# Kernel optimization log

Hardware: AMD Instinct MI355X
Metric: run time of the kernel (lower is better)

The kernel has to match this reference:

```python
import jax, jax.numpy as jnp
import numpy as np
import math

B, N, K, M = 8, 512, 128, 100

def _lin(k, fi, fo):
    kw, kb = jax.random.split(k)
    return (jax.random.normal(kw, (fi, fo), jnp.float32) / np.sqrt(fi).astype(np.float32),
            jax.random.normal(kb, (fo,), jnp.float32) * 0.01)

def setup_inputs() -> dict:
    key = jax.random.key(0)
    ks = jax.random.split(key, 10)
    xyz = jax.random.uniform(ks[0], (B, N, K, 3), jnp.float32, minval=0.5, maxval=2.8)
    counts = jax.random.randint(ks[1], (B, N), 32, K + 1)
    # padded neighbor list: valid neighbors first (flag=1), padding zeros after -> break == mask
    flags = (jnp.arange(K)[None, None, :] < counts[:, :, None]).astype(jnp.float32)
    image_dR = jnp.concatenate([xyz, flags[..., None]], axis=-1)  # [B,N,K,4]
    ew0, eb0 = _lin(ks[2], 1, 25)
    ew1, eb1 = _lin(ks[3], 25, 50)
    ew2, eb2 = _lin(ks[4], 50, M)
    fw0, fb0 = _lin(ks[5], 16 * M, 240)
    fw1, fb1 = _lin(ks[6], 240, 240)
    fw2, fb2 = _lin(ks[7], 240, 240)
    fw3, fb3 = _lin(ks[8], 240, 1)
    return dict(image_dR=image_dR, ew0=ew0, eb0=eb0, ew1=ew1, eb1=eb1, ew2=ew2, eb2=eb2,
                fw0=fw0, fb0=fb0, fw1=fw1, fb1=fb1, fw2=fw2, fb2=fb2, fw3=fw3, fb3=fb3)

def reference(image_dR, ew0, eb0, ew1, eb1, ew2, eb2, fw0, fb0, fw1, fb1, fw2, fb2, fw3, fb3):
    list_neigh = image_dR[..., 3]            # [B,N,K] neighbor flag
    xyz = image_dR[..., :3]                  # [B,N,K,3]
    Rij = jnp.sum(xyz * xyz, axis=-1)        # NOTE: original overwrites sqrt -> squared distance
    mask = list_neigh > 0
    lt10 = Rij < 10.0
    b1 = mask & lt10
    b2 = (~lt10) & (Rij < 25.0)              # cosine branch ignores mask (faithful)
    safe = jnp.where(Rij == 0.0, 1.0, Rij)
    S = jnp.where(b1, 1.0 / safe,
                  jnp.where(b2, 0.5 * jnp.cos(math.pi * (Rij - 10.0) / 15.0) + 0.5, 0.0))
    coef = jnp.where(mask, S / safe, 0.0)    # per-neighbor scaling for xyz channels
    Ri = jnp.concatenate([S[..., None], coef[..., None] * xyz], axis=-1)  # [B,N,K,4]
    # embedding net on scalar S_Rij
    h = jnp.tanh(S[..., None] @ ew0 + eb0)
    h = jnp.tanh(h @ ew1 + eb1)
    G = jnp.tanh(h @ ew2 + eb2)              # [B,N,K,M]
    G16 = G[..., :16]
    tmpA = jnp.einsum('bnjm,bnjf->bnmf', G16, Ri)   # [B,N,16,4]
    tmpB = jnp.einsum('bnjf,bnjm->bnfm', Ri, G)     # [B,N,4,M]
    DR = jnp.einsum('bnmf,bnfh->bnmh', tmpA, tmpB).reshape(image_dR.shape[0], image_dR.shape[1], -1)
    h = jnp.tanh(DR @ fw0 + fb0)
    h = jnp.tanh(h @ fw1 + fb1)
    h = jnp.tanh(h @ fw2 + fb2)
    Ei = h @ fw3 + fb3                       # [B,N,1]
    Etot = jnp.sum(Ei, axis=1)               # [B,1]
    return Etot, Ei
```

## Files before the change

kernel.cpp:

```cpp
#include <hip/hip_runtime.h>
#include <hip/hip_bf16.h>
#include <math.h>

#define B_ 8
#define N_ 512
#define K_ 128
#define M_ 100
#define NPAIR (B_*N_)
#define DRLEN 1600
#define F0 240
#define NPAD 256

#define NLUT 2048
#define LUT_STRIDE 128
#define SMAX 1.5f
#define EPB 8

using bf16x8 = __attribute__((ext_vector_type(8))) __bf16;
using f32x4  = __attribute__((ext_vector_type(4))) float;

static __device__ __forceinline__ float tanh_f(float x){
  float xc = fminf(fmaxf(x, -15.f), 15.f);
  float e = __expf(2.f*xc);
  return __fdividef(e - 1.f, e + 1.f);
}

__global__ __launch_bounds__(256) void lut_build_par(
    const float* __restrict__ ew0, const float* __restrict__ eb0,
    const float* __restrict__ ew1, const float* __restrict__ eb1,
    const float* __restrict__ ew2, const float* __restrict__ eb2,
    float* __restrict__ T)
{
  __shared__ float sh0[EPB][26];
  __shared__ float sh1[EPB][52];
  const int e0 = blockIdx.x * EPB;
  const int t = threadIdx.x;

  if (t < EPB*25){
    int e = t / 25, c = t % 25;
    float S = (float)(e0 + e) * (SMAX / (float)(NLUT - 1));
    sh0[e][c] = tanh_f(fmaf(S, ew0[c], eb0[c]));
  }
  __syncthreads();

  for (int o = t; o < EPB*50; o += 256){
    int e = o / 50, c = o % 50;
    float a = eb1[c], b = 0.f;
    #pragma unroll
    for (int k = 0; k < 24; k += 2){
      a = fmaf(sh0[e][k],   ew1[k*50 + c],     a);
      b = fmaf(sh0[e][k+1], ew1[(k+1)*50 + c], b);
    }
    a = fmaf(sh0[e][24], ew1[24*50 + c], a);
    sh1[e][c] = tanh_f(a + b);
  }
  __syncthreads();

  for (int o = t; o < EPB*M_; o += 256){
    int e = o / M_, c = o % M_;
    float a = eb2[c], b = 0.f;
    #pragma unroll
    for (int k = 0; k < 50; k += 2){
      a = fmaf(sh1[e][k],   ew2[k*M_ + c],     a);
      b = fmaf(sh1[e][k+1], ew2[(k+1)*M_ + c], b);
    }
    T[(size_t)(e0 + e)*LUT_STRIDE + c] = tanh_f(a + b);
  }
}

__global__ __launch_bounds__(256) void prep_w0t(
    const float* __restrict__ src, __hip_bfloat16* __restrict__ dst)
{
  __shared__ float tile[64][65];
  const int k0 = blockIdx.x * 64;
  const int n0 = blockIdx.y * 64;
  const int tc = threadIdx.x & 63, tr = threadIdx.x >> 6;

  #pragma unroll
  for (int i = 0; i < 16; i += 1){
    int r = i*4 + tr;
    int n = n0 + tc;
    tile[r][tc] = (n < F0) ? src[(size_t)(k0 + r)*F0 + n] : 0.f;
  }
  __syncthreads();
  #pragma unroll
  for (int i = 0; i < 16; i += 1){
    int r = i*4 + tr;
    dst[(size_t)(n0 + r)*DRLEN + k0 + tc] = __float2bfloat16(tile[tc][r]);
  }
}

__global__ __launch_bounds__(256) void prep_small(
    const float* __restrict__ fw1, const float* __restrict__ fw2,
    const float* __restrict__ fb0, const float* __restrict__ fb1,
    const float* __restrict__ fb2,
    __hip_bfloat16* __restrict__ W1T, __hip_bfloat16* __restrict__ W2T,
    float* __restrict__ b0p, float* __restrict__ b1p, float* __restrict__ b2p)
{
  int idx = blockIdx.x*256 + threadIdx.x;
  if (idx < NPAD*NPAD){
    int n = idx / NPAD, k = idx % NPAD;
    W1T[idx] = __float2bfloat16((n < F0 && k < F0) ? fw1[(size_t)k*F0 + n] : 0.f);
  } else if (idx < 2*NPAD*NPAD){
    int j = idx - NPAD*NPAD;
    int n = j / NPAD, k = j % NPAD;
    W2T[j] = __float2bfloat16((n < F0 && k < F0) ? fw2[(size_t)k*F0 + n] : 0.f);
  } else if (idx < 2*NPAD*NPAD + 3*NPAD){
    int j = idx - 2*NPAD*NPAD;
    int which = j / NPAD, c = j % NPAD;
    const float* s = (which == 0) ? fb0 : (which == 1) ? fb1 : fb2;
    float* d = (which == 0) ? b0p : (which == 1) ? b1p : b2p;
    d[c] = (c < F0) ? s[c] : 0.f;
  }
}

__global__ __launch_bounds__(128) void embed_kernel(
    const float* __restrict__ img, const float* __restrict__ T,
    __hip_bfloat16* __restrict__ DR)
{
  __shared__ float4 sRi[K_];
  __shared__ float2 sJW[K_];
  __shared__ float  sB[4][M_];

  const int pair = blockIdx.x;
  const int t = threadIdx.x;

  {
    float4 v = *(const float4*)(img + ((size_t)pair*K_ + t)*4);
    float x = v.x, y = v.y, z = v.z, fl = v.w;
    float R = fmaf(x, x, fmaf(y, y, z*z));
    bool mask = fl > 0.f;
    bool lt10 = R < 10.f;
    float safe = (R == 0.f) ? 1.f : R;
    float Sc = 0.5f*cosf(0.20943951023931953f*(R - 10.f)) + 0.5f;
    float S;
    if (mask && lt10)            S = 1.f/safe;
    else if (!lt10 && R < 25.f)  S = Sc;
    else                         S = 0.f;
    float coef = mask ? S/safe : 0.f;
    sRi[t] = make_float4(S, coef*x, coef*y, coef*z);

    float fidx = fminf(S, SMAX) * ((float)(NLUT - 1) / SMAX);
    float fi = floorf(fidx);
    int i = (int)fi;
    float w = fidx - fi;
    if (i > NLUT - 2){ i = NLUT - 2; w = 1.f; }
    sJW[t] = make_float2((float)i, w);
  }
  __syncthreads();

  if (t < M_){
    const int m = t;
    float a0 = 0.f, a1 = 0.f, a2 = 0.f, a3 = 0.f;
    #pragma unroll 4
    for (int j = 0; j < K_; j++){
      float2 jw = sJW[j];
      float4 ri = sRi[j];
      const float* r0 = T + (size_t)((int)jw.x) * LUT_STRIDE + m;
      float t0 = r0[0];
      float t1 = r0[LUT_STRIDE];
      float g = fmaf(jw.y, t1 - t0, t0);
      a0 = fmaf(ri.x, g, a0);
      a1 = fmaf(ri.y, g, a1);
      a2 = fmaf(ri.z, g, a2);
      a3 = fmaf(ri.w, g, a3);
    }
    sB[0][m] = a0; sB[1][m] = a1; sB[2][m] = a2; sB[3][m] = a3;
  }
  __syncthreads();

  __hip_bfloat16* drp = DR + (size_t)pair*DRLEN;
  for (int o = t; o < DRLEN; o += 128){
    int m = o / M_, h = o % M_;
    float d = sB[0][m]*sB[0][h] + sB[1][m]*sB[1][h]
            + sB[2][m]*sB[2][h] + sB[3][m]*sB[3][h];
    drp[o] = __float2bfloat16(d);
  }
}

template<int KK, int NITER>
__global__ __launch_bounds__(256) void gemm_lds(
    const __hip_bfloat16* __restrict__ A_, const __hip_bfloat16* __restrict__ Bt_,
    const float* __restrict__ bias, __hip_bfloat16* __restrict__ Y)
{
  __shared__ __align__(16) __bf16 As[2][64][72];
  __shared__ __align__(16) __bf16 Bs[2][64][72];

  const __bf16* A  = (const __bf16*)A_;
  const __bf16* Bt = (const __bf16*)Bt_;
  const int tid = threadIdx.x;
  const int lane = tid & 63, wave = tid >> 6;
  const int wm = wave & 1, wn = wave >> 1;
  const int l15 = lane & 15, q = lane >> 4;
  const int row0 = blockIdx.x * 64;
  const int col0 = blockIdx.y * 64;

  int arow[2], ac8[2]; size_t aoff[2], boff[2];
  #pragma unroll
  for (int i = 0; i < 2; i++){
    int cid = tid + i*256; arow[i] = cid >> 3; ac8[i] = cid & 7;
    aoff[i] = (size_t)(row0 + arow[i])*KK + ac8[i]*8;
    boff[i] = (size_t)(col0 + arow[i])*KK + ac8[i]*8;
  }

  bf16x8 Ar[2][2], Br[2][2];

  #pragma unroll
  for (int i = 0; i < 2; i++) Ar[0][i] = *(const bf16x8*)(A + aoff[i]);
  #pragma unroll
  for (int i = 0; i < 2; i++) Br[0][i] = *(const bf16x8*)(Bt + boff[i]);
  #pragma unroll
  for (int i = 0; i < 2; i++) *(bf16x8*)&As[0][arow[i]][ac8[i]*8] = Ar[0][i];
  #pragma unroll
  for (int i = 0; i < 2; i++) *(bf16x8*)&Bs[0][arow[i]][ac8[i]*8] = Br[0][i];
  #pragma unroll
  for (int i = 0; i < 2; i++) Ar[1][i] = *(const bf16x8*)(A + aoff[i] + 64);
  #pragma unroll
  for (int i = 0; i < 2; i++) Br[1][i] = *(const bf16x8*)(Bt + boff[i] + 64);
  __syncthreads();

  f32x4 acc[2][2] = {};

  #pragma unroll
  for (int it = 0; it < NITER; it++){
    const int buf = it & 1;
    #pragma unroll
    for (int ks = 0; ks < 2; ks++){
      bf16x8 a0 = *(const bf16x8*)&As[buf][wm*32 +      l15][ks*32 + q*8];
      bf16x8 a1 = *(const bf16x8*)&As[buf][wm*32 + 16 + l15][ks*32 + q*8];
      bf16x8 b0 = *(const bf16x8*)&Bs[buf][wn*32 +      l15][ks*32 + q*8];
      bf16x8 b1 = *(const bf16x8*)&Bs[buf][wn*32 + 16 + l15][ks*32 + q*8];
      acc[0][0] = __builtin_amdgcn_mfma_f32_16x16x32_bf16(a0, b0, acc[0][0], 0,0,0);
      acc[1][0] = __builtin_amdgcn_mfma_f32_16x16x32_bf16(a1, b0, acc[1][0], 0,0,0);
      acc[0][1] = __builtin_amdgcn_mfma_f32_16x16x32_bf16(a0, b1, acc[0][1], 0,0,0);
      acc[1][1] = __builtin_amdgcn_mfma_f32_16x16x32_bf16(a1, b1, acc[1][1], 0,0,0);
    }
    if (it + 1 < NITER){
      const int nb = buf ^ 1;
      const int set = (it + 1) & 1;
      #pragma unroll
      for (int i = 0; i < 2; i++) *(bf16x8*)&As[nb][arow[i]][ac8[i]*8] = Ar[set][i];
      #pragma unroll
      for (int i = 0; i < 2; i++) *(bf16x8*)&Bs[nb][arow[i]][ac8[i]*8] = Br[set][i];
      if (it + 2 < NITER){
        const int s2 = it & 1;
        const size_t k2 = (size_t)(it + 2) * 64;
        #pragma unroll
        for (int i = 0; i < 2; i++) Ar[s2][i] = *(const bf16x8*)(A + aoff[i] + k2);
        #pragma unroll
        for (int i = 0; i < 2; i++) Br[s2][i] = *(const bf16x8*)(Bt + boff[i] + k2);
      }
      __syncthreads();
    }
  }

  #pragma unroll
  for (int i = 0; i < 2; i++){
    #pragma unroll
    for (int j = 0; j < 2; j++){
      int c = col0 + wn*32 + j*16 + l15;
      float bs = bias[c];
      #pragma unroll
      for (int r = 0; r < 4; r++){
        int rr = row0 + wm*32 + i*16 + q*4 + r;
        float v = tanh_f(acc[i][j][r] + bs);
        Y[(size_t)rr*NPAD + c] = __float2bfloat16(v);
      }
    }
  }
}

__global__ __launch_bounds__(256) void gemv_out(
    const __hip_bfloat16* __restrict__ H, const float* __restrict__ w3,
    const float* __restrict__ b3, float* __restrict__ Ei,
    float* __restrict__ outEi)
{
  int row  = (blockIdx.x * 256 + threadIdx.x) >> 6;
  int lane = threadIdx.x & 63;
  const __hip_bfloat16* hp = H + (size_t)row * NPAD;
  float a = 0.f;
  for (int k = lane; k < F0; k += 64) a = fmaf(__bfloat162float(hp[k]), w3[k], a);
  #pragma unroll
  for (int off = 32; off; off >>= 1) a += __shfl_down(a, off, 64);
  if (lane == 0){
    float e = a + b3[0];
    Ei[row] = e;
    outEi[row] = e;
  }
}

__global__ __launch_bounds__(256) void etot_k(
    const float* __restrict__ Ei, float* __restrict__ outE)
{
  int b = blockIdx.x;
  int t = threadIdx.x;
  float s = Ei[b*N_ + t] + Ei[b*N_ + 256 + t];
  #pragma unroll
  for (int off = 32; off; off >>= 1) s += __shfl_down(s, off, 64);
  __shared__ float ws[4];
  if ((t & 63) == 0) ws[t >> 6] = s;
  __syncthreads();
  if (t == 0) outE[b] = ws[0] + ws[1] + ws[2] + ws[3];
}

extern "C" void kernel_launch(void* const* d_in, const int* in_sizes, int n_in,
                              void* d_out, int out_size, void* d_ws, size_t ws_size,
                              hipStream_t stream)
{
  const float* img = (const float*)d_in[0];
  const float* ew0 = (const float*)d_in[1];
  const float* eb0 = (const float*)d_in[2];
  const float* ew1 = (const float*)d_in[3];
  const float* eb1 = (const float*)d_in[4];
  const float* ew2 = (const float*)d_in[5];
  const float* eb2 = (const float*)d_in[6];
  const float* fw0 = (const float*)d_in[7];
  const float* fb0 = (const float*)d_in[8];
  const float* fw1 = (const float*)d_in[9];
  const float* fb1 = (const float*)d_in[10];
  const float* fw2 = (const float*)d_in[11];
  const float* fb2 = (const float*)d_in[12];
  const float* fw3 = (const float*)d_in[13];
  const float* fb3 = (const float*)d_in[14];

  char* w = (char*)d_ws;
  __hip_bfloat16* DRb = (__hip_bfloat16*)(w);
  __hip_bfloat16* H1b = (__hip_bfloat16*)(w + 13107200);
  __hip_bfloat16* H2b = (__hip_bfloat16*)(w + 15204352);
  __hip_bfloat16* H3b = (__hip_bfloat16*)(w + 17301504);
  __hip_bfloat16* W0T = (__hip_bfloat16*)(w + 19398656);
  __hip_bfloat16* W1T = (__hip_bfloat16*)(w + 20217856);
  __hip_bfloat16* W2T = (__hip_bfloat16*)(w + 20348928);
  float* b0p = (float*)(w + 20480000);
  float* b1p = (float*)(w + 20481024);
  float* b2p = (float*)(w + 20482048);
  float* LUT = (float*)(w + 20483072);
  float* Ei  = (float*)(w + 21531648);

  float* out = (float*)d_out;

  prep_w0t<<<dim3(DRLEN/64, NPAD/64), 256, 0, stream>>>(fw0, W0T);
  const int small_elems = 2*NPAD*NPAD + 3*NPAD;
  prep_small<<<(small_elems + 255)/256, 256, 0, stream>>>(
      fw1, fw2, fb0, fb1, fb2, W1T, W2T, b0p, b1p, b2p);

  lut_build_par<<<NLUT/EPB, 256, 0, stream>>>(ew0, eb0, ew1, eb1, ew2, eb2, LUT);
  embed_kernel<<<NPAIR, 128, 0, stream>>>(img, LUT, DRb);

  dim3 gg(NPAIR/64, NPAD/64);
  gemm_lds<DRLEN, 25><<<gg, 256, 0, stream>>>(DRb, W0T, b0p, H1b);
  gemm_lds<NPAD,   4><<<gg, 256, 0, stream>>>(H1b, W1T, b1p, H2b);
  gemm_lds<NPAD,   4><<<gg, 256, 0, stream>>>(H2b, W2T, b2p, H3b);

  gemv_out<<<NPAIR/4, 256, 0, stream>>>(H3b, fw3, fb3, Ei, out + 8);
  etot_k<<<B_, 256, 0, stream>>>(Ei, out);
}
```

Before: 149.9 us.

## Fuse prep kernels into one launch and interleave LUT neighbor entries

Merges the W0 transpose, small weight/bias prep and LUT build kernels into a single launch dispatched by block index, cutting launch overhead. The LUT now stores each entry paired with its successor as float2, so the embedding loop performs one 8-byte gather instead of two strided loads and uses a precomputed integer offset. This doubles LUT memory and adds a scattered write for the neighbor slot.

Measured after the change: 152.2 us. No clear change (+1.5%).

```diff
diff --git a/kernel.cpp b/kernel.cpp
--- a/kernel.cpp
+++ b/kernel.cpp
@@ -12,7 +12,7 @@
 #define NPAD 256
 
 #define NLUT 2048
-#define LUT_STRIDE 128
+#define LUT2_STRIDE 128
 #define SMAX 1.5f
 #define EPB 8
 
@@ -25,101 +25,106 @@
   return __fdividef(e - 1.f, e + 1.f);
 }
 
-__global__ __launch_bounds__(256) void lut_build_par(
+#define W0T_BLOCKS 100
+#define SMALL_ELEMS (2*NPAD*NPAD + 3*NPAD)
+#define SMALL_BLOCKS ((SMALL_ELEMS + 255)/256)
+#define LUT_BLOCKS (NLUT/EPB)
+
+__global__ __launch_bounds__(256) void prep_fused(
+    const float* __restrict__ fw0, const float* __restrict__ fw1,
+    const float* __restrict__ fw2,
+    const float* __restrict__ fb0, const float* __restrict__ fb1,
+    const float* __restrict__ fb2,
     const float* __restrict__ ew0, const float* __restrict__ eb0,
     const float* __restrict__ ew1, const float* __restrict__ eb1,
     const float* __restrict__ ew2, const float* __restrict__ eb2,
-    float* __restrict__ T)
-{
+    __hip_bfloat16* __restrict__ W0T, __hip_bfloat16* __restrict__ W1T,
+    __hip_bfloat16* __restrict__ W2T,
+    float* __restrict__ b0p, float* __restrict__ b1p, float* __restrict__ b2p,
+    float2* __restrict__ T2)
+{
+  __shared__ float tile[64][65];
   __shared__ float sh0[EPB][26];
   __shared__ float sh1[EPB][52];
-  const int e0 = blockIdx.x * EPB;
+  const int bb = blockIdx.x;
   const int t = threadIdx.x;
 
-  if (t < EPB*25){
-    int e = t / 25, c = t % 25;
-    float S = (float)(e0 + e) * (SMAX / (float)(NLUT - 1));
-    sh0[e][c] = tanh_f(fmaf(S, ew0[c], eb0[c]));
-  }
-  __syncthreads();
-
-  for (int o = t; o < EPB*50; o += 256){
-    int e = o / 50, c = o % 50;
-    float a = eb1[c], b = 0.f;
+  if (bb < W0T_BLOCKS){
+    const int k0 = (bb % 25) * 64;
+    const int n0 = (bb / 25) * 64;
+    const int tc = t & 63, tr = t >> 6;
     #pragma unroll
-    for (int k = 0; k < 24; k += 2){
-      a = fmaf(sh0[e][k],   ew1[k*50 + c],     a);
-      b = fmaf(sh0[e][k+1], ew1[(k+1)*50 + c], b);
-    }
-    a = fmaf(sh0[e][24], ew1[24*50 + c], a);
-    sh1[e][c] = tanh_f(a + b);
-  }
-  __syncthreads();
-
-  for (int o = t; o < EPB*M_; o += 256){
-    int e = o / M_, c = o % M_;
-    float a = eb2[c], b = 0.f;
+    for (int i = 0; i < 16; i++){
+      int r = i*4 + tr;
+      int n = n0 + tc;
+      tile[r][tc] = (n < F0) ? fw0[(size_t)(k0 + r)*F0 + n] : 0.f;
+    }
+    __syncthreads();
     #pragma unroll
-    for (int k = 0; k < 50; k += 2){
-      a = fmaf(sh1[e][k],   ew2[k*M_ + c],     a);
-      b = fmaf(sh1[e][k+1], ew2[(k+1)*M_ + c], b);
-    }
-    T[(size_t)(e0 + e)*LUT_STRIDE + c] = tanh_f(a + b);
-  }
-}
-
-__global__ __launch_bounds__(256) void prep_w0t(
-    const float* __restrict__ src, __hip_bfloat16* __restrict__ dst)
-{
-  __shared__ float tile[64][65];
-  const int k0 = blockIdx.x * 64;
-  const int n0 = blockIdx.y * 64;
-  const int tc = threadIdx.x & 63, tr = threadIdx.x >> 6;
-
-  #pragma unroll
-  for (int i = 0; i < 16; i += 1){
-    int r = i*4 + tr;
-    int n = n0 + tc;
-    tile[r][tc] = (n < F0) ? src[(size_t)(k0 + r)*F0 + n] : 0.f;
-  }
-  __syncthreads();
-  #pragma unroll
-  for (int i = 0; i < 16; i += 1){
-    int r = i*4 + tr;
-    dst[(size_t)(n0 + r)*DRLEN + k0 + tc] = __float2bfloat16(tile[tc][r]);
-  }
-}
-
-__global__ __launch_bounds__(256) void prep_small(
-    const float* __restrict__ fw1, const float* __restrict__ fw2,
-    const float* __restrict__ fb0, const float* __restrict__ fb1,
-    const float* __restrict__ fb2,
-    __hip_bfloat16* __restrict__ W1T, __hip_bfloat16* __restrict__ W2T,
-    float* __restrict__ b0p, float* __restrict__ b1p, float* __restrict__ b2p)
-{
-  int idx = blockIdx.x*256 + threadIdx.x;
-  if (idx < NPAD*NPAD){
-    int n = idx / NPAD, k = idx % NPAD;
-    W1T[idx] = __float2bfloat16((n < F0 && k < F0) ? fw1[(size_t)k*F0 + n] : 0.f);
-  } else if (idx < 2*NPAD*NPAD){
-    int j = idx - NPAD*NPAD;
-    int n = j / NPAD, k = j % NPAD;
-    W2T[j] = __float2bfloat16((n < F0 && k < F0) ? fw2[(size_t)k*F0 + n] : 0.f);
-  } else if (idx < 2*NPAD*NPAD + 3*NPAD){
-    int j = idx - 2*NPAD*NPAD;
-    int which = j / NPAD, c = j % NPAD;
-    const float* s = (which == 0) ? fb0 : (which == 1) ? fb1 : fb2;
-    float* d = (which == 0) ? b0p : (which == 1) ? b1p : b2p;
-    d[c] = (c < F0) ? s[c] : 0.f;
+    for (int i = 0; i < 16; i++){
+      int r = i*4 + tr;
+      W0T[(size_t)(n0 + r)*DRLEN + k0 + tc] = __float2bfloat16(tile[tc][r]);
+    }
+  } else if (bb < W0T_BLOCKS + SMALL_BLOCKS){
+    int idx = (bb - W0T_BLOCKS)*256 + t;
+    if (idx < NPAD*NPAD){
+      int n = idx / NPAD, k = idx % NPAD;
+      W1T[idx] = __float2bfloat16((n < F0 && k < F0) ? fw1[(size_t)k*F0 + n] : 0.f);
+    } else if (idx < 2*NPAD*NPAD){
+      int j = idx - NPAD*NPAD;
+      int n = j / NPAD, k = j % NPAD;
+      W2T[j] = __float2bfloat16((n < F0 && k < F0) ? fw2[(size_t)k*F0 + n] : 0.f);
+    } else if (idx < SMALL_ELEMS){
+      int j = idx - 2*NPAD*NPAD;
+      int which = j / NPAD, c = j % NPAD;
+      const float* s = (which == 0) ? fb0 : (which == 1) ? fb1 : fb2;
+      float* d = (which == 0) ? b0p : (which == 1) ? b1p : b2p;
+      d[c] = (c < F0) ? s[c] : 0.f;
+    }
+  } else {
+    const int e0 = (bb - W0T_BLOCKS - SMALL_BLOCKS) * EPB;
+    if (t < EPB*25){
+      int e = t / 25, c = t % 25;
+      float S = (float)(e0 + e) * (SMAX / (float)(NLUT - 1));
+      sh0[e][c] = tanh_f(fmaf(S, ew0[c], eb0[c]));
+    }
+    __syncthreads();
+    for (int o = t; o < EPB*50; o += 256){
+      int e = o / 50, c = o % 50;
+      float a = eb1[c], b = 0.f;
+      #pragma unroll
+      for (int k = 0; k < 24; k += 2){
+        a = fmaf(sh0[e][k],   ew1[k*50 + c],     a);
+        b = fmaf(sh0[e][k+1], ew1[(k+1)*50 + c], b);
+      }
+      a = fmaf(sh0[e][24], ew1[24*50 + c], a);
+      sh1[e][c] = tanh_f(a + b);
+    }
+    __syncthreads();
+    for (int o = t; o < EPB*M_; o += 256){
+      int e = o / M_, c = o % M_;
+      float a = eb2[c], b = 0.f;
+      #pragma unroll
+      for (int k = 0; k < 50; k += 2){
+        a = fmaf(sh1[e][k],   ew2[k*M_ + c],     a);
+        b = fmaf(sh1[e][k+1], ew2[(k+1)*M_ + c], b);
+      }
+      float g = tanh_f(a + b);
+      int ge = e0 + e;
+      T2[(size_t)ge*LUT2_STRIDE + c].x = g;
+      if (ge > 0)
+        T2[(size_t)(ge-1)*LUT2_STRIDE + c].y = g;
+    }
   }
 }
 
 __global__ __launch_bounds__(128) void embed_kernel(
-    const float* __restrict__ img, const float* __restrict__ T,
+    const float* __restrict__ img, const float2* __restrict__ T2,
     __hip_bfloat16* __restrict__ DR)
 {
   __shared__ float4 sRi[K_];
-  __shared__ float2 sJW[K_];
+  __shared__ int    sJ[K_];
+  __shared__ float  sW[K_];
   __shared__ float  sB[4][M_];
 
   const int pair = blockIdx.x;
@@ -145,7 +150,8 @@
     int i = (int)fi;
     float w = fidx - fi;
     if (i > NLUT - 2){ i = NLUT - 2; w = 1.f; }
-    sJW[t] = make_float2((float)i, w);
+    sJ[t] = i * LUT2_STRIDE;
+    sW[t] = w;
   }
   __syncthreads();
 
@@ -154,12 +160,11 @@
     float a0 = 0.f, a1 = 0.f, a2 = 0.f, a3 = 0.f;
     #pragma unroll 4
     for (int j = 0; j < K_; j++){
-      float2 jw = sJW[j];
+      int off = sJ[j];
+      float w = sW[j];
       float4 ri = sRi[j];
-      const float* r0 = T + (size_t)((int)jw.x) * LUT_STRIDE + m;
-      float t0 = r0[0];
-      float t1 = r0[LUT_STRIDE];
-      float g = fmaf(jw.y, t1 - t0, t0);
+      float2 tv = T2[off + m];
+      float g = fmaf(w, tv.y - tv.x, tv.x);
       a0 = fmaf(ri.x, g, a0);
       a1 = fmaf(ri.y, g, a1);
       a2 = fmaf(ri.z, g, a2);
@@ -334,18 +339,17 @@
   float* b0p = (float*)(w + 20480000);
   float* b1p = (float*)(w + 20481024);
   float* b2p = (float*)(w + 20482048);
-  float* LUT = (float*)(w + 20483072);
-  float* Ei  = (float*)(w + 21531648);
+  float2* LUT2 = (float2*)(w + 20483072);
+  float* Ei  = (float*)(w + 22580224);
 
   float* out = (float*)d_out;
 
-  prep_w0t<<<dim3(DRLEN/64, NPAD/64), 256, 0, stream>>>(fw0, W0T);
-  const int small_elems = 2*NPAD*NPAD + 3*NPAD;
-  prep_small<<<(small_elems + 255)/256, 256, 0, stream>>>(
-      fw1, fw2, fb0, fb1, fb2, W1T, W2T, b0p, b1p, b2p);
-
-  lut_build_par<<<NLUT/EPB, 256, 0, stream>>>(ew0, eb0, ew1, eb1, ew2, eb2, LUT);
-  embed_kernel<<<NPAIR, 128, 0, stream>>>(img, LUT, DRb);
+  prep_fused<<<W0T_BLOCKS + SMALL_BLOCKS + LUT_BLOCKS, 256, 0, stream>>>(
+      fw0, fw1, fw2, fb0, fb1, fb2,
+      ew0, eb0, ew1, eb1, ew2, eb2,
+      W0T, W1T, W2T, b0p, b1p, b2p, LUT2);
+
+  embed_kernel<<<NPAIR, 128, 0, stream>>>(img, LUT2, DRb);
 
   dim3 gg(NPAIR/64, NPAD/64);
   gemm_lds<DRLEN, 25><<<gg, 256, 0, stream>>>(DRb, W0T, b0p, H1b);
```
